# Performance work log

Measured on AMD Instinct MI355X. Metric: run time of the kernel, lower is better.

The kernel has to match this reference:

```python
import jax, jax.numpy as jnp
import numpy as np

N, C, K = 65536, 128, 16

def setup_inputs() -> dict:
    key = jax.random.key(0)
    ks = jax.random.split(key, 16)
    def w(k, i, o):
        return jax.random.normal(k, (i, o), dtype=jnp.float32) / np.sqrt(i)
    inp = {
        "x": jax.random.normal(ks[0], (N, C), dtype=jnp.float32),
        "coords": jax.random.normal(ks[1], (N, 3), dtype=jnp.float32) * 10.0,
        "neighbor_idx": jax.random.randint(ks[2], (N, K), 0, N, dtype=jnp.int32),
        # linear_top / linear_down (1x1 Minkowski convs, BN folded into affine)
        "W_top": w(ks[3], C, C), "b_top": jnp.zeros((C,), jnp.float32),
        "W_down": w(ks[4], C, C), "b_down": jnp.zeros((C,), jnp.float32),
        # phi (query), psi (key), alpha (value) 1x1 convs
        "W_phi": w(ks[5], C, C), "b_phi": jnp.zeros((C,), jnp.float32),
        "W_psi": w(ks[6], C, C), "b_psi": jnp.zeros((C,), jnp.float32),
        "W_alpha": w(ks[7], C, C), "b_alpha": jnp.zeros((C,), jnp.float32),
        # delta: positional-encoding MLP on relative xyz (3 -> C -> C)
        "W_d1": w(ks[8], 3, C), "b_d1": jnp.zeros((C,), jnp.float32),
        "W_d2": w(ks[9], C, C), "b_d2": jnp.zeros((C,), jnp.float32),
        # gamma: attention MLP (C -> C -> C), vector attention
        "W_g1": w(ks[10], C, C), "b_g1": jnp.zeros((C,), jnp.float32),
        "W_g2": w(ks[11], C, C), "b_g2": jnp.zeros((C,), jnp.float32),
    }
    return inp

def reference(x, coords, W_top, b_top, W_down, b_down, W_phi, b_phi, W_psi, b_psi,
              W_alpha, b_alpha, W_d1, b_d1, W_d2, b_d2, W_g1, b_g1, W_g2, b_g2,
              neighbor_idx):
    # linear_top
    h = x @ W_top + b_top                                  # (N, C)
    phi = h @ W_phi + b_phi                                # (N, C) query
    psi = h @ W_psi + b_psi                                # (N, C) key
    alpha = h @ W_alpha + b_alpha                          # (N, C) value
    # gather neighbor features / coords (irregular access)
    nb_psi = psi[neighbor_idx]                             # (N, K, C)
    nb_alpha = alpha[neighbor_idx]                         # (N, K, C)
    rel = coords[:, None, :] - coords[neighbor_idx]        # (N, K, 3)
    # delta: relative positional encoding MLP
    pos = jax.nn.relu(rel @ W_d1 + b_d1) @ W_d2 + b_d2     # (N, K, C)
    # vector attention: gamma(phi_i - psi_j + delta)
    attn_in = phi[:, None, :] - nb_psi + pos               # (N, K, C)
    logits = jax.nn.relu(attn_in @ W_g1 + b_g1) @ W_g2 + b_g2
    w = jax.nn.softmax(logits, axis=1)                     # softmax over K neighbors
    y = jnp.sum(w * (nb_alpha + pos), axis=1)              # (N, C)
    # linear_down + residual
    return y @ W_down + b_down + x
```

## Files before the change

### kernel.cpp

```cpp
#include <hip/hip_runtime.h>
#include <math.h>

#define C 128
#define K 16
#define M 4
#define ROWS 64

typedef unsigned short ushort_t;
typedef unsigned int u32;
typedef float f32x4 __attribute__((ext_vector_type(4)));
typedef _Float16 f16x8 __attribute__((ext_vector_type(8)));

union U8h { _Float16 h[8]; uint4 u; };

__device__ __forceinline__ float f16tof(ushort_t b) {
    _Float16 h = __builtin_bit_cast(_Float16, b); return (float)h;
}
__device__ __forceinline__ ushort_t ftof16(float f) {
    _Float16 h = (_Float16)f; return __builtin_bit_cast(ushort_t, h);
}
__device__ __forceinline__ f32x4 mfma16(f16x8 a, f16x8 b, f32x4 c) {
    return __builtin_amdgcn_mfma_f32_16x16x32_f16(a, b, c, 0, 0, 0);
}

__global__ __launch_bounds__(128) void k_prep(
    const float* __restrict__ s0, const float* __restrict__ s1,
    const float* __restrict__ s2, const float* __restrict__ s3,
    ushort_t* __restrict__ d0, ushort_t* __restrict__ d1,
    ushort_t* __restrict__ d2, ushort_t* __restrict__ d3)
{
    const int m = blockIdx.x >> 7, n = blockIdx.x & 127, e = threadIdx.x;
    const float* s = (m==0) ? s0 : (m==1) ? s1 : (m==2) ? s2 : s3;
    ushort_t*   d = (m==0) ? d0 : (m==1) ? d1 : (m==2) ? d2 : d3;
    d[n*C + e] = ftof16(s[e*C + n]);
}

__global__ __launch_bounds__(512) void k_qkv2(
    const float* __restrict__ x,
    const ushort_t* __restrict__ WTt, const float* __restrict__ bt,
    const ushort_t* __restrict__ WTp, const float* __restrict__ bp,
    const ushort_t* __restrict__ WTs, const float* __restrict__ bs,
    const ushort_t* __restrict__ WTa, const float* __restrict__ ba,
    ushort_t* __restrict__ phiB, ushort_t* __restrict__ psiB,
    ushort_t* __restrict__ alfB)
{
    __shared__ ushort_t sX[64*C];
    __shared__ ushort_t sH[64*C];
    const int tid = threadIdx.x, lane = tid & 63, wv = tid >> 6;
    const int ncol = (wv<<4) + (lane&15), arow = lane&15;
    const int kgrp = lane>>4, krow0 = kgrp<<3;
    const int r0 = blockIdx.x * 64;

    {
        const int rX = tid>>3, cX = (tid&7)<<4;
        const float* xp = &x[(size_t)(r0+rX)*C + cX];
        #pragma unroll
        for (int hf = 0; hf < 2; ++hf) {
            const float4 a  = *(const float4*)&xp[hf*8 + 0];
            const float4 b2 = *(const float4*)&xp[hf*8 + 4];
            U8h v;
            v.h[0]=(_Float16)a.x;  v.h[1]=(_Float16)a.y;
            v.h[2]=(_Float16)a.z;  v.h[3]=(_Float16)a.w;
            v.h[4]=(_Float16)b2.x; v.h[5]=(_Float16)b2.y;
            v.h[6]=(_Float16)b2.z; v.h[7]=(_Float16)b2.w;
            const int col = cX + hf*8;
            *(uint4*)&sX[(rX<<7) + (col ^ ((rX&7)<<3))] = v.u;
        }
    }
    __syncthreads();

    {
        f16x8 bf[4]; f32x4 hacc[4];
        #pragma unroll
        for (int kk = 0; kk < 4; ++kk)
            bf[kk] = *(const f16x8*)&WTt[(size_t)ncol*C + (kk<<5) + krow0];
        #pragma unroll
        for (int m = 0; m < 4; ++m) hacc[m] = (f32x4){0.f,0.f,0.f,0.f};
        __builtin_amdgcn_s_setprio(1);
        #pragma unroll
        for (int m = 0; m < 4; ++m)
            #pragma unroll
            for (int kk = 0; kk < 4; ++kk) {
                const int row = (m<<4) + arow;
                const f16x8 af = *(const f16x8*)&sX[(row<<7) + (((kk<<5)+krow0) ^ ((arow&7)<<3))];
                hacc[m] = mfma16(af, bf[kk], hacc[m]);
            }
        __builtin_amdgcn_s_setprio(0);
        const float btc = bt[ncol];
        #pragma unroll
        for (int m = 0; m < 4; ++m)
            #pragma unroll
            for (int r = 0; r < 4; ++r) {
                const int row = (m<<4) + (kgrp<<2) + r;
                sH[(row<<7) + (ncol ^ ((row&7)<<3))] = ftof16(hacc[m][r] + btc);
            }
    }
    __syncthreads();

#define OGEMM(WT_, b_, o_)                                                    \
    {                                                                         \
        f16x8 wf[4]; f32x4 oacc[4];                                           \
        _Pragma("unroll")                                                     \
        for (int kk = 0; kk < 4; ++kk)                                        \
            wf[kk] = *(const f16x8*)&WT_[(size_t)ncol*C + (kk<<5) + krow0];   \
        _Pragma("unroll")                                                     \
        for (int m = 0; m < 4; ++m) oacc[m] = (f32x4){0.f,0.f,0.f,0.f};      \
        __builtin_amdgcn_s_setprio(1);                                        \
        _Pragma("unroll")                                                     \
        for (int m = 0; m < 4; ++m)                                           \
            _Pragma("unroll")                                                 \
            for (int kk = 0; kk < 4; ++kk) {                                  \
                const int row = (m<<4) + arow;                                \
                const f16x8 af = *(const f16x8*)&sH[(row<<7) + (((kk<<5)+krow0) ^ ((arow&7)<<3))]; \
                oacc[m] = mfma16(af, wf[kk], oacc[m]);                        \
            }                                                                 \
        __builtin_amdgcn_s_setprio(0);                                        \
        const float bc = b_[ncol];                                            \
        _Pragma("unroll")                                                     \
        for (int m = 0; m < 4; ++m)                                           \
            _Pragma("unroll")                                                 \
            for (int r = 0; r < 4; ++r) {                                     \
                const int row = (m<<4) + (kgrp<<2) + r;                       \
                o_[(size_t)(r0+row)*C + ncol] = ftof16(oacc[m][r] + bc);      \
            }                                                                 \
    }
    OGEMM(WTp, bp, phiB)
    OGEMM(WTs, bs, psiB)
    OGEMM(WTa, ba, alfB)
#undef OGEMM
}

__global__ __launch_bounds__(512, 4) void k_attn11(
    const ushort_t* __restrict__ phiB, const ushort_t* __restrict__ psiB,
    const ushort_t* __restrict__ alfB,
    const float* __restrict__ coords, const int* __restrict__ nidx,
    const float* __restrict__ Wd1, const float* __restrict__ bd1,
    const ushort_t* __restrict__ WTd2, const float* __restrict__ bd2,
    const ushort_t* __restrict__ WTg1, const float* __restrict__ bg1,
    const ushort_t* __restrict__ WTg2,
    ushort_t* __restrict__ yB,
    int ngroups, int gpb)
{
    __shared__ ushort_t sT[ROWS*C];
    __shared__ ushort_t sA[ROWS*C];
    __shared__ ushort_t sP[ROWS*C];
    __shared__ float    sW1b[512];

    const int tid  = threadIdx.x, lane = tid & 63, wv = tid >> 6;
    const int ncol = (wv<<4) + (lane&15);
    const int arow = lane & 15;
    const int kgrp = lane >> 4, krow0 = kgrp << 3;
    const int rb   = kgrp << 2;
    const int grow = tid >> 3;
    const int gpt  = grow >> 4;
    const int gk   = grow & 15;
    const int gc   = (tid & 7) << 4;

    const int g0 = blockIdx.x * gpb;
    if (g0 >= ngroups) return;
    const int gend = (g0 + gpb < ngroups) ? (g0 + gpb) : ngroups;

    for (int i = tid; i < 512; i += 256)
        if (i < 512) sW1b[i] = (i < 384) ? Wd1[i] : bd1[i - 384];

    const float bd2c = bd2[ncol];
    const float bg1c = bg1[ncol];

    __syncthreads();

    for (int g = g0; g < gend; ++g) {
        const int p0 = g * M;

        {
            const int pt = p0 + gpt;
            const int jt = nidx[(size_t)pt*K + gk];
            const float rx = coords[(size_t)pt*3+0] - coords[(size_t)jt*3+0];
            const float ry = coords[(size_t)pt*3+1] - coords[(size_t)jt*3+1];
            const float rz = coords[(size_t)pt*3+2] - coords[(size_t)jt*3+2];
            #pragma unroll
            for (int s = 0; s < 2; ++s) {
                U8h h;
                #pragma unroll
                for (int z = 0; z < 8; ++z) {
                    const int c = gc + (s<<3) + z;
                    float t = fmaf(rx, sW1b[c],
                              fmaf(ry, sW1b[128+c],
                              fmaf(rz, sW1b[256+c], sW1b[384+c])));
                    h.h[z] = (_Float16)fmaxf(t, 0.f);
                }
                *(uint4*)&sT[(grow<<7) + ((gc + (s<<3)) ^ ((grow&7)<<3))] = h.u;
            }
        }
        __syncthreads();

        {
            f32x4 acc[M];
            #pragma unroll
            for (int m = 0; m < M; ++m) acc[m] = (f32x4){0.f,0.f,0.f,0.f};
            __builtin_amdgcn_s_setprio(1);
            #pragma unroll
            for (int kk = 0; kk < 4; ++kk) {
                const f16x8 w = *(const f16x8*)&WTd2[(size_t)ncol*C + (kk<<5) + krow0];
                #pragma unroll
                for (int m = 0; m < M; ++m) {
                    const f16x8 af = *(const f16x8*)&sT[(((m<<4)+arow)<<7) + (((kk<<5)+krow0) ^ ((arow&7)<<3))];
                    acc[m] = mfma16(af, w, acc[m]);
                }
            }
            __builtin_amdgcn_s_setprio(0);

            #pragma unroll
            for (int m = 0; m < M; ++m) {
                const float ph = f16tof(phiB[(size_t)(p0+m)*C + ncol]);
                const int4 j4 = *(const int4*)&nidx[(size_t)(p0+m)*K + rb];
                #pragma unroll
                for (int r = 0; r < 4; ++r) {
                    const int j = (r==0) ? j4.x : (r==1) ? j4.y : (r==2) ? j4.z : j4.w;
                    const float ps = f16tof(psiB[(size_t)j*C + ncol]);
                    const int row = (m<<4) + rb + r;
                    const int si  = (row<<7) + (ncol ^ ((row&7)<<3));
                    const float pv = acc[m][r] + bd2c;
                    sP[si] = ftof16(pv);
                    sA[si] = ftof16(ph - ps + pv);
                }
            }
        }
        __syncthreads();

        {
            f32x4 acc[M];
            #pragma unroll
            for (int m = 0; m < M; ++m) acc[m] = (f32x4){0.f,0.f,0.f,0.f};
            __builtin_amdgcn_s_setprio(1);
            #pragma unroll
            for (int kk = 0; kk < 4; ++kk) {
                const f16x8 w = *(const f16x8*)&WTg1[(size_t)ncol*C + (kk<<5) + krow0];
                #pragma unroll
                for (int m = 0; m < M; ++m) {
                    const f16x8 af = *(const f16x8*)&sA[(((m<<4)+arow)<<7) + (((kk<<5)+krow0) ^ ((arow&7)<<3))];
                    acc[m] = mfma16(af, w, acc[m]);
                }
            }
            __builtin_amdgcn_s_setprio(0);
            #pragma unroll
            for (int m = 0; m < M; ++m)
                #pragma unroll
                for (int r = 0; r < 4; ++r) {
                    const int row = (m<<4) + rb + r;
                    sT[(row<<7) + (ncol ^ ((row&7)<<3))] =
                        ftof16(fmaxf(acc[m][r] + bg1c, 0.f));
                }
        }
        __syncthreads();

        {
            f32x4 acc[M];
            #pragma unroll
            for (int m = 0; m < M; ++m) acc[m] = (f32x4){0.f,0.f,0.f,0.f};
            __builtin_amdgcn_s_setprio(1);
            #pragma unroll
            for (int kk = 0; kk < 4; ++kk) {
                const f16x8 w = *(const f16x8*)&WTg2[(size_t)ncol*C + (kk<<5) + krow0];
                #pragma unroll
                for (int m = 0; m < M; ++m) {
                    const f16x8 af = *(const f16x8*)&sT[(((m<<4)+arow)<<7) + (((kk<<5)+krow0) ^ ((arow&7)<<3))];
                    acc[m] = mfma16(af, w, acc[m]);
                }
            }
            __builtin_amdgcn_s_setprio(0);

            #pragma unroll
            for (int m = 0; m < M; ++m) {
                const f32x4 l = acc[m];
                float mx = fmaxf(fmaxf(l[0], l[1]), fmaxf(l[2], l[3]));
                mx = fmaxf(mx, __shfl_xor(mx, 16));
                mx = fmaxf(mx, __shfl_xor(mx, 32));
                const float e0 = __expf(l[0]-mx), e1 = __expf(l[1]-mx);
                const float e2 = __expf(l[2]-mx), e3 = __expf(l[3]-mx);
                float den = e0 + e1 + e2 + e3;
                den += __shfl_xor(den, 16);
                den += __shfl_xor(den, 32);
                const float inv = 1.0f / den;
                const int4 j4 = *(const int4*)&nidx[(size_t)(p0+m)*K + rb];
                float yp = 0.f;
                #pragma unroll
                for (int r = 0; r < 4; ++r) {
                    const int j = (r==0) ? j4.x : (r==1) ? j4.y : (r==2) ? j4.z : j4.w;
                    const float av = f16tof(alfB[(size_t)j*C + ncol]);
                    const int row = (m<<4) + rb + r;
                    const float pr = f16tof(sP[(row<<7) + (ncol ^ ((row&7)<<3))]);
                    const float ee = (r==0) ? e0 : (r==1) ? e1 : (r==2) ? e2 : e3;
                    yp = fmaf(ee, av + pr, yp);
                }
                yp *= inv;
                yp += __shfl_xor(yp, 16);
                yp += __shfl_xor(yp, 32);
                if (lane < 16)
                    yB[(size_t)(p0+m)*C + ncol] = ftof16(yp);
            }
        }
        __syncthreads();
    }
}

__global__ __launch_bounds__(512) void k_down(
    const ushort_t* __restrict__ yB,
    const ushort_t* __restrict__ WTdn, const float* __restrict__ bdn,
    const float* __restrict__ x, float* __restrict__ out)
{
    __shared__ ushort_t sY[64*C];
    const int tid = threadIdx.x, lane = tid & 63, wv = tid >> 6;
    const int ncol = (wv<<4) + (lane&15), arow = lane&15;
    const int kgrp = lane>>4, krow0 = kgrp<<3;
    const int r0 = blockIdx.x * 64;

    {
        const int rY = tid>>3, cY = (tid&7)<<4;
        #pragma unroll
        for (int hf = 0; hf < 2; ++hf) {
            const uint4 v = *(const uint4*)&yB[(size_t)(r0+rY)*C + cY + hf*8];
            *(uint4*)&sY[(rY<<7) + ((cY + hf*8) ^ ((rY&7)<<3))] = v;
        }
    }
    __syncthreads();

    f16x8 wf[4]; f32x4 oacc[4];
    #pragma unroll
    for (int kk = 0; kk < 4; ++kk)
        wf[kk] = *(const f16x8*)&WTdn[(size_t)ncol*C + (kk<<5) + krow0];
    #pragma unroll
    for (int m = 0; m < 4; ++m) oacc[m] = (f32x4){0.f,0.f,0.f,0.f};
    __builtin_amdgcn_s_setprio(1);
    #pragma unroll
    for (int m = 0; m < 4; ++m)
        #pragma unroll
        for (int kk = 0; kk < 4; ++kk) {
            const int row = (m<<4) + arow;
            const f16x8 af = *(const f16x8*)&sY[(row<<7) + (((kk<<5)+krow0) ^ ((arow&7)<<3))];
            oacc[m] = mfma16(af, wf[kk], oacc[m]);
        }
    __builtin_amdgcn_s_setprio(0);
    const float bc = bdn[ncol];
    #pragma unroll
    for (int m = 0; m < 4; ++m)
        #pragma unroll
        for (int r = 0; r < 4; ++r) {
            const int row = (m<<4) + (kgrp<<2) + r;
            const size_t idx = (size_t)(r0+row)*C + ncol;
            out[idx] = oacc[m][r] + bc + x[idx];
        }
}

extern "C" void kernel_launch(void* const* d_in, const int* in_sizes, int n_in,
                              void* d_out, int out_size, void* d_ws, size_t ws_size,
                              hipStream_t stream)
{
    const float* x      = (const float*)d_in[0];
    const float* coords = (const float*)d_in[1];
    const int*   nidx   = (const int*)d_in[2];
    const float* W_top  = (const float*)d_in[3];
    const float* b_top  = (const float*)d_in[4];
    const float* W_down = (const float*)d_in[5];
    const float* b_down = (const float*)d_in[6];
    const float* W_phi  = (const float*)d_in[7];
    const float* b_phi  = (const float*)d_in[8];
    const float* W_psi  = (const float*)d_in[9];
    const float* b_psi  = (const float*)d_in[10];
    const float* W_alpha= (const float*)d_in[11];
    const float* b_alpha= (const float*)d_in[12];
    const float* W_d1   = (const float*)d_in[13];
    const float* b_d1   = (const float*)d_in[14];
    const float* W_d2   = (const float*)d_in[15];
    const float* b_d2   = (const float*)d_in[16];
    const float* W_g1   = (const float*)d_in[17];
    const float* b_g1   = (const float*)d_in[18];
    const float* W_g2   = (const float*)d_in[19];
    const float* b_g2   = (const float*)d_in[20];
    (void)b_g2;

    const int N = in_sizes[0] / C;

    ushort_t* WTt  = (ushort_t*)d_ws;
    ushort_t* WTp  = WTt  + C*C;
    ushort_t* WTs  = WTp  + C*C;
    ushort_t* WTa  = WTs  + C*C;
    ushort_t* WTd2 = WTa  + C*C;
    ushort_t* WTg1 = WTd2 + C*C;
    ushort_t* WTg2 = WTg1 + C*C;
    ushort_t* WTdn = WTg2 + C*C;
    ushort_t* phiB = WTdn + C*C;
    ushort_t* psiB = phiB + (size_t)N*C;
    ushort_t* alfB = psiB + (size_t)N*C;
    ushort_t* yB   = alfB + (size_t)N*C;
    float* out = (float*)d_out;

    hipLaunchKernelGGL(k_prep, dim3(4*C), dim3(C), 0, stream,
        W_top, W_phi, W_psi, W_alpha, WTt, WTp, WTs, WTa);
    hipLaunchKernelGGL(k_prep, dim3(4*C), dim3(C), 0, stream,
        W_d2, W_g1, W_g2, W_down, WTd2, WTg1, WTg2, WTdn);

    hipLaunchKernelGGL(k_qkv2, dim3(N / 64), dim3(512), 0, stream,
        x, WTt, b_top, WTp, b_phi, WTs, b_psi, WTa, b_alpha,
        phiB, psiB, alfB);

    const int ngroups = N / M;
    const int NBLK = 2048;
    const int gpb = (ngroups + NBLK - 1) / NBLK;
    hipLaunchKernelGGL(k_attn11, dim3(NBLK), dim3(512), 0, stream,
        phiB, psiB, alfB, coords, nidx,
        W_d1, b_d1, WTd2, b_d2, WTg1, b_g1, WTg2,
        yB, ngroups, gpb);

    hipLaunchKernelGGL(k_down, dim3(N / 64), dim3(512), 0, stream,
        yB, WTdn, b_down, x, out);
}
```

Measured before the change: 578.8 us.

## Restructure attention kernel with 32x32 MFMA tiles and register-held gathers

The attention kernel now processes 8 points (128 neighbor rows) per iteration using 32x32x16 MFMA tiles. Each wave owns 32 rows and 64 columns. The pos, psi and alpha values stay in registers instead of being staged through a third shared buffer, and the psi/alpha gathers are issued up front to overlap with the positional MLP. The softmax and weighted sum are done per lane across rows with fewer shuffles. The grid is cut to 256 blocks at 2 waves-per-SIMD occupancy, trading parallelism for reuse and more register pressure. The change also alters the swizzle index in the other GEMMs (arow&7 to row&7), which has the same value since m<<4 is a multiple of 8.

```diff
diff --git a/kernel.cpp b/kernel.cpp
--- a/kernel.cpp
+++ b/kernel.cpp
@@ -3,12 +3,13 @@
 
 #define C 128
 #define K 16
-#define M 4
-#define ROWS 64
+#define GP 8
+#define GROWS 128
 
 typedef unsigned short ushort_t;
 typedef unsigned int u32;
 typedef float f32x4 __attribute__((ext_vector_type(4)));
+typedef float f32x16 __attribute__((ext_vector_type(16)));
 typedef _Float16 f16x8 __attribute__((ext_vector_type(8)));
 
 union U8h { _Float16 h[8]; uint4 u; };
@@ -22,6 +23,14 @@
 __device__ __forceinline__ f32x4 mfma16(f16x8 a, f16x8 b, f32x4 c) {
     return __builtin_amdgcn_mfma_f32_16x16x32_f16(a, b, c, 0, 0, 0);
 }
+__device__ __forceinline__ f32x16 mfma32(f16x8 a, f16x8 b, f32x16 c) {
+    return __builtin_amdgcn_mfma_f32_32x32x16_f16(a, b, c, 0, 0, 0);
+}
+
+#define GETJ(r) ((r) < 4 ? ((r)==0?ja0.x:(r)==1?ja0.y:(r)==2?ja0.z:ja0.w)      \
+               : (r) < 8 ? ((r)==4?jb0.x:(r)==5?jb0.y:(r)==6?jb0.z:jb0.w)      \
+               : (r) <12 ? ((r)==8?ja1.x:(r)==9?ja1.y:(r)==10?ja1.z:ja1.w)     \
+                         : ((r)==12?jb1.x:(r)==13?jb1.y:(r)==14?jb1.z:jb1.w))
 
 __global__ __launch_bounds__(128) void k_prep(
     const float* __restrict__ s0, const float* __restrict__ s1,
@@ -82,7 +91,7 @@
             #pragma unroll
             for (int kk = 0; kk < 4; ++kk) {
                 const int row = (m<<4) + arow;
-                const f16x8 af = *(const f16x8*)&sX[(row<<7) + (((kk<<5)+krow0) ^ ((arow&7)<<3))];
+                const f16x8 af = *(const f16x8*)&sX[(row<<7) + (((kk<<5)+krow0) ^ ((row&7)<<3))];
                 hacc[m] = mfma16(af, bf[kk], hacc[m]);
             }
         __builtin_amdgcn_s_setprio(0);
@@ -111,7 +120,7 @@
             _Pragma("unroll")                                                 \
             for (int kk = 0; kk < 4; ++kk) {                                  \
                 const int row = (m<<4) + arow;                                \
-                const f16x8 af = *(const f16x8*)&sH[(row<<7) + (((kk<<5)+krow0) ^ ((arow&7)<<3))]; \
+                const f16x8 af = *(const f16x8*)&sH[(row<<7) + (((kk<<5)+krow0) ^ ((row&7)<<3))]; \
                 oacc[m] = mfma16(af, wf[kk], oacc[m]);                        \
             }                                                                 \
         __builtin_amdgcn_s_setprio(0);                                        \
@@ -130,7 +139,7 @@
 #undef OGEMM
 }
 
-__global__ __launch_bounds__(512, 4) void k_attn11(
+__global__ __launch_bounds__(512, 2) void k_attn13(
     const ushort_t* __restrict__ phiB, const ushort_t* __restrict__ psiB,
     const ushort_t* __restrict__ alfB,
     const float* __restrict__ coords, const int* __restrict__ nidx,
@@ -141,163 +150,180 @@
     ushort_t* __restrict__ yB,
     int ngroups, int gpb)
 {
-    __shared__ ushort_t sT[ROWS*C];
-    __shared__ ushort_t sA[ROWS*C];
-    __shared__ ushort_t sP[ROWS*C];
+    __shared__ ushort_t sT[GROWS*C];
+    __shared__ ushort_t sA[GROWS*C];
     __shared__ float    sW1b[512];
 
-    const int tid  = threadIdx.x, lane = tid & 63, wv = tid >> 6;
-    const int ncol = (wv<<4) + (lane&15);
-    const int arow = lane & 15;
-    const int kgrp = lane >> 4, krow0 = kgrp << 3;
-    const int rb   = kgrp << 2;
-    const int grow = tid >> 3;
-    const int gpt  = grow >> 4;
-    const int gk   = grow & 15;
-    const int gc   = (tid & 7) << 4;
+    const int tid   = threadIdx.x, lane = tid & 63, wid = tid >> 6;
+    const int chunk = wid >> 1;
+    const int ch0   = (wid & 1) << 6;
+    const int lcol  = lane & 31;
+    const int hi    = lane >> 5;
+    const int col0  = ch0 + lcol;
+    const int col1  = col0 + 32;
+    const int arow  = (chunk << 5) + lcol;
+    const int asw   = (arow & 7) << 3;
+    const int trow  = tid >> 2;
+    const int tch   = (tid & 3) << 5;
+
+    if (tid < 512) sW1b[tid] = (tid < 384) ? Wd1[tid] : bd1[tid - 384];
+
+    const float bd2c0 = bd2[col0], bd2c1 = bd2[col1];
+    const float bg1c0 = bg1[col0], bg1c1 = bg1[col1];
 
     const int g0 = blockIdx.x * gpb;
     if (g0 >= ngroups) return;
     const int gend = (g0 + gpb < ngroups) ? (g0 + gpb) : ngroups;
 
-    for (int i = tid; i < 512; i += 256)
-        if (i < 512) sW1b[i] = (i < 384) ? Wd1[i] : bd1[i - 384];
-
-    const float bd2c = bd2[ncol];
-    const float bg1c = bg1[ncol];
-
     __syncthreads();
 
     for (int g = g0; g < gend; ++g) {
-        const int p0 = g * M;
+        const int p0 = g * GP;
+
+        const int pt0 = p0 + (chunk<<1), pt1 = pt0 + 1;
+        const int4 ja0 = *(const int4*)&nidx[(size_t)pt0*K + (hi<<2)];
+        const int4 jb0 = *(const int4*)&nidx[(size_t)pt0*K + 8 + (hi<<2)];
+        const int4 ja1 = *(const int4*)&nidx[(size_t)pt1*K + (hi<<2)];
+        const int4 jb1 = *(const int4*)&nidx[(size_t)pt1*K + 8 + (hi<<2)];
+
+        ushort_t psv0[16], psv1[16], alv0[16], alv1[16];
+        #pragma unroll
+        for (int r = 0; r < 16; ++r) {
+            const int j = GETJ(r);
+            psv0[r] = psiB[(size_t)j*C + col0];
+            psv1[r] = psiB[(size_t)j*C + col1];
+            alv0[r] = alfB[(size_t)j*C + col0];
+            alv1[r] = alfB[(size_t)j*C + col1];
+        }
+        const float ph00 = f16tof(phiB[(size_t)pt0*C + col0]);
+        const float ph01 = f16tof(phiB[(size_t)pt0*C + col1]);
+        const float ph10 = f16tof(phiB[(size_t)pt1*C + col0]);
+        const float ph11 = f16tof(phiB[(size_t)pt1*C + col1]);
 
         {
-            const int pt = p0 + gpt;
-            const int jt = nidx[(size_t)pt*K + gk];
+            const int pt = p0 + (trow>>4);
+            const int jt = nidx[(size_t)pt*K + (trow&15)];
             const float rx = coords[(size_t)pt*3+0] - coords[(size_t)jt*3+0];
             const float ry = coords[(size_t)pt*3+1] - coords[(size_t)jt*3+1];
             const float rz = coords[(size_t)pt*3+2] - coords[(size_t)jt*3+2];
             #pragma unroll
-            for (int s = 0; s < 2; ++s) {
+            for (int s = 0; s < 4; ++s) {
                 U8h h;
                 #pragma unroll
                 for (int z = 0; z < 8; ++z) {
-                    const int c = gc + (s<<3) + z;
+                    const int c = tch + (s<<3) + z;
                     float t = fmaf(rx, sW1b[c],
                               fmaf(ry, sW1b[128+c],
                               fmaf(rz, sW1b[256+c], sW1b[384+c])));
                     h.h[z] = (_Float16)fmaxf(t, 0.f);
                 }
-                *(uint4*)&sT[(grow<<7) + ((gc + (s<<3)) ^ ((grow&7)<<3))] = h.u;
+                *(uint4*)&sT[(trow<<7) + ((tch + (s<<3)) ^ ((trow&7)<<3))] = h.u;
             }
         }
         __syncthreads();
 
+        f32x16 pos0 = {0}, pos1 = {0};
         {
-            f32x4 acc[M];
-            #pragma unroll
-            for (int m = 0; m < M; ++m) acc[m] = (f32x4){0.f,0.f,0.f,0.f};
             __builtin_amdgcn_s_setprio(1);
             #pragma unroll
-            for (int kk = 0; kk < 4; ++kk) {
-                const f16x8 w = *(const f16x8*)&WTd2[(size_t)ncol*C + (kk<<5) + krow0];
-                #pragma unroll
-                for (int m = 0; m < M; ++m) {
-                    const f16x8 af = *(const f16x8*)&sT[(((m<<4)+arow)<<7) + (((kk<<5)+krow0) ^ ((arow&7)<<3))];
-                    acc[m] = mfma16(af, w, acc[m]);
+            for (int kk = 0; kk < 8; ++kk) {
+                const int kc = (kk<<4) + (hi<<3);
+                const f16x8 a  = *(const f16x8*)&sT[(arow<<7) + (kc ^ asw)];
+                const f16x8 w0 = *(const f16x8*)&WTd2[(size_t)col0*C + kc];
+                const f16x8 w1 = *(const f16x8*)&WTd2[(size_t)col1*C + kc];
+                pos0 = mfma32(a, w0, pos0);
+                pos1 = mfma32(a, w1, pos1);
+            }
+            __builtin_amdgcn_s_setprio(0);
+            #pragma unroll
+            for (int r = 0; r < 16; ++r) {
+                const int lrow = (r&3) + (((r>>2)&1)<<3) + ((r>>3)<<4) + (hi<<2);
+                const int grow = (chunk<<5) + lrow;
+                const int sw   = (grow&7)<<3;
+                const float pv0 = pos0[r] + bd2c0;
+                const float pv1 = pos1[r] + bd2c1;
+                pos0[r] = pv0; pos1[r] = pv1;
+                const float ph_0 = (r < 8) ? ph00 : ph10;
+                const float ph_1 = (r < 8) ? ph01 : ph11;
+                const u32 v0 = ftof16(ph_0 - f16tof(psv0[r]) + pv0);
+                const u32 v1 = ftof16(ph_1 - f16tof(psv1[r]) + pv1);
+                const u32 p0v = (u32)__shfl_xor((int)v0, 1);
+                const u32 p1v = (u32)__shfl_xor((int)v1, 1);
+                if (!(lane&1)) {
+                    *(u32*)&sA[(grow<<7) + ((col0&~1) ^ sw)] = v0 | (p0v<<16);
+                    *(u32*)&sA[(grow<<7) + ((col1&~1) ^ sw)] = v1 | (p1v<<16);
                 }
             }
+        }
+        __syncthreads();
+
+        {
+            f32x16 u0 = {0}, u1 = {0};
+            __builtin_amdgcn_s_setprio(1);
+            #pragma unroll
+            for (int kk = 0; kk < 8; ++kk) {
+                const int kc = (kk<<4) + (hi<<3);
+                const f16x8 a  = *(const f16x8*)&sA[(arow<<7) + (kc ^ asw)];
+                const f16x8 w0 = *(const f16x8*)&WTg1[(size_t)col0*C + kc];
+                const f16x8 w1 = *(const f16x8*)&WTg1[(size_t)col1*C + kc];
+                u0 = mfma32(a, w0, u0);
+                u1 = mfma32(a, w1, u1);
+            }
             __builtin_amdgcn_s_setprio(0);
-
-            #pragma unroll
-            for (int m = 0; m < M; ++m) {
-                const float ph = f16tof(phiB[(size_t)(p0+m)*C + ncol]);
-                const int4 j4 = *(const int4*)&nidx[(size_t)(p0+m)*K + rb];
-                #pragma unroll
-                for (int r = 0; r < 4; ++r) {
-                    const int j = (r==0) ? j4.x : (r==1) ? j4.y : (r==2) ? j4.z : j4.w;
-                    const float ps = f16tof(psiB[(size_t)j*C + ncol]);
-                    const int row = (m<<4) + rb + r;
-                    const int si  = (row<<7) + (ncol ^ ((row&7)<<3));
-                    const float pv = acc[m][r] + bd2c;
-                    sP[si] = ftof16(pv);
-                    sA[si] = ftof16(ph - ps + pv);
+            #pragma unroll
+            for (int r = 0; r < 16; ++r) {
+                const int lrow = (r&3) + (((r>>2)&1)<<3) + ((r>>3)<<4) + (hi<<2);
+                const int grow = (chunk<<5) + lrow;
+                const int sw   = (grow&7)<<3;
+                const u32 v0 = ftof16(fmaxf(u0[r] + bg1c0, 0.f));
+                const u32 v1 = ftof16(fmaxf(u1[r] + bg1c1, 0.f));
+                const u32 p0v = (u32)__shfl_xor((int)v0, 1);
+                const u32 p1v = (u32)__shfl_xor((int)v1, 1);
+                if (!(lane&1)) {
+                    *(u32*)&sT[(grow<<7) + ((col0&~1) ^ sw)] = v0 | (p0v<<16);
+                    *(u32*)&sT[(grow<<7) + ((col1&~1) ^ sw)] = v1 | (p1v<<16);
                 }
             }
         }
         __syncthreads();
 
         {
-            f32x4 acc[M];
-            #pragma unroll
-            for (int m = 0; m < M; ++m) acc[m] = (f32x4){0.f,0.f,0.f,0.f};
+            f32x16 lg0 = {0}, lg1 = {0};
             __builtin_amdgcn_s_setprio(1);
             #pragma unroll
-            for (int kk = 0; kk < 4; ++kk) {
-                const f16x8 w = *(const f16x8*)&WTg1[(size_t)ncol*C + (kk<<5) + krow0];
-                #pragma unroll
-                for (int m = 0; m < M; ++m) {
-                    const f16x8 af = *(const f16x8*)&sA[(((m<<4)+arow)<<7) + (((kk<<5)+krow0) ^ ((arow&7)<<3))];
-                    acc[m] = mfma16(af, w, acc[m]);
-                }
+            for (int kk = 0; kk < 8; ++kk) {
+                const int kc = (kk<<4) + (hi<<3);
+                const f16x8 a  = *(const f16x8*)&sT[(arow<<7) + (kc ^ asw)];
+                const f16x8 w0 = *(const f16x8*)&WTg2[(size_t)col0*C + kc];
+                const f16x8 w1 = *(const f16x8*)&WTg2[(size_t)col1*C + kc];
+                lg0 = mfma32(a, w0, lg0);
+                lg1 = mfma32(a, w1, lg1);
             }
             __builtin_amdgcn_s_setprio(0);
-            #pragma unroll
-            for (int m = 0; m < M; ++m)
-                #pragma unroll
-                for (int r = 0; r < 4; ++r) {
-                    const int row = (m<<4) + rb + r;
-                    sT[(row<<7) + (ncol ^ ((row&7)<<3))] =
-                        ftof16(fmaxf(acc[m][r] + bg1c, 0.f));
-                }
-        }
-        __syncthreads();
-
-        {
-            f32x4 acc[M];
-            #pragma unroll
-            for (int m = 0; m < M; ++m) acc[m] = (f32x4){0.f,0.f,0.f,0.f};
-            __builtin_amdgcn_s_setprio(1);
-            #pragma unroll
-            for (int kk = 0; kk < 4; ++kk) {
-                const f16x8 w = *(const f16x8*)&WTg2[(size_t)ncol*C + (kk<<5) + krow0];
-                #pragma unroll
-                for (int m = 0; m < M; ++m) {
-                    const f16x8 af = *(const f16x8*)&sT[(((m<<4)+arow)<<7) + (((kk<<5)+krow0) ^ ((arow&7)<<3))];
-                    acc[m] = mfma16(af, w, acc[m]);
-                }
-            }
-            __builtin_amdgcn_s_setprio(0);
-
-            #pragma unroll
-            for (int m = 0; m < M; ++m) {
-                const f32x4 l = acc[m];
-                float mx = fmaxf(fmaxf(l[0], l[1]), fmaxf(l[2], l[3]));
-                mx = fmaxf(mx, __shfl_xor(mx, 16));
-                mx = fmaxf(mx, __shfl_xor(mx, 32));
-                const float e0 = __expf(l[0]-mx), e1 = __expf(l[1]-mx);
-                const float e2 = __expf(l[2]-mx), e3 = __expf(l[3]-mx);
-                float den = e0 + e1 + e2 + e3;
-                den += __shfl_xor(den, 16);
-                den += __shfl_xor(den, 32);
-                const float inv = 1.0f / den;
-                const int4 j4 = *(const int4*)&nidx[(size_t)(p0+m)*K + rb];
-                float yp = 0.f;
-                #pragma unroll
-                for (int r = 0; r < 4; ++r) {
-                    const int j = (r==0) ? j4.x : (r==1) ? j4.y : (r==2) ? j4.z : j4.w;
-                    const float av = f16tof(alfB[(size_t)j*C + ncol]);
-                    const int row = (m<<4) + rb + r;
-                    const float pr = f16tof(sP[(row<<7) + (ncol ^ ((row&7)<<3))]);
-                    const float ee = (r==0) ? e0 : (r==1) ? e1 : (r==2) ? e2 : e3;
-                    yp = fmaf(ee, av + pr, yp);
-                }
-                yp *= inv;
-                yp += __shfl_xor(yp, 16);
-                yp += __shfl_xor(yp, 32);
-                if (lane < 16)
-                    yB[(size_t)(p0+m)*C + ncol] = ftof16(yp);
-            }
+
+#define SOFTMAX_Y(LG, POS, ALV, RB, PT, COLX)                                 \
+            {                                                                 \
+                float mx = -1e30f;                                            \
+                _Pragma("unroll")                                             \
+                for (int r = 0; r < 8; ++r) mx = fmaxf(mx, LG[RB + r]);       \
+                mx = fmaxf(mx, __shfl_xor(mx, 32));                           \
+                float den = 0.f, yp = 0.f;                                    \
+                _Pragma("unroll")                                             \
+                for (int r = 0; r < 8; ++r) {                                 \
+                    const float e = __expf(LG[RB + r] - mx);                  \
+                    den += e;                                                 \
+                    yp  = fmaf(e, f16tof(ALV[RB + r]) + POS[RB + r], yp);     \
+                }                                                             \
+                den += __shfl_xor(den, 32);                                   \
+                yp  += __shfl_xor(yp, 32);                                    \
+                yp  /= den;                                                   \
+                if (hi == 0) yB[(size_t)(PT)*C + (COLX)] = ftof16(yp);        \
+            }
+            SOFTMAX_Y(lg0, pos0, alv0, 0, pt0, col0)
+            SOFTMAX_Y(lg1, pos1, alv1, 0, pt0, col1)
+            SOFTMAX_Y(lg0, pos0, alv0, 8, pt1, col0)
+            SOFTMAX_Y(lg1, pos1, alv1, 8, pt1, col1)
+#undef SOFTMAX_Y
         }
         __syncthreads();
     }
@@ -336,7 +362,7 @@
         #pragma unroll
         for (int kk = 0; kk < 4; ++kk) {
             const int row = (m<<4) + arow;
-            const f16x8 af = *(const f16x8*)&sY[(row<<7) + (((kk<<5)+krow0) ^ ((arow&7)<<3))];
+            const f16x8 af = *(const f16x8*)&sY[(row<<7) + (((kk<<5)+krow0) ^ ((row&7)<<3))];
             oacc[m] = mfma16(af, wf[kk], oacc[m]);
         }
     __builtin_amdgcn_s_setprio(0);
@@ -403,10 +429,10 @@
         x, WTt, b_top, WTp, b_phi, WTs, b_psi, WTa, b_alpha,
         phiB, psiB, alfB);
 
-    const int ngroups = N / M;
-    const int NBLK = 2048;
+    const int ngroups = N / GP;
+    const int NBLK = 256;
     const int gpb = (ngroups + NBLK - 1) / NBLK;
-    hipLaunchKernelGGL(k_attn11, dim3(NBLK), dim3(512), 0, stream,
+    hipLaunchKernelGGL(k_attn13, dim3(NBLK), dim3(512), 0, stream,
         phiB, psiB, alfB, coords, nidx,
         W_d1, b_d1, WTd2, b_d2, WTg1, b_g1, WTg2,
         yB, ngroups, gpb);
```

Result: slower. 1.022 ms (+76.6%).
